# Optimization experiments

Measured on AMD Instinct MI355X. Metric: run time of the kernel, lower is better.

The kernel has to match this reference:

```python
import jax, jax.numpy as jnp
import numpy as np

D_MODEL = 1024
NUM_HEAD = 16
CHUNK = 64
NGROUPS = 2
D_HEAD = D_MODEL // NUM_HEAD
NEG = -1e30


def setup_inputs() -> dict:
    key = jax.random.key(0)
    ks = jax.random.split(key, 4)
    bs, seq = 2, 4096
    proj_dim = 3 * D_MODEL + 2 * NGROUPS * D_HEAD
    hidden = jax.random.normal(ks[0], (bs, seq, D_MODEL), jnp.float32)
    W_in = jax.random.normal(ks[1], (D_MODEL, proj_dim), jnp.float32) * (D_MODEL ** -0.5)
    # torch init: uniform_(1, chunk_size-1) then log
    gate_bias = jnp.log(jax.random.uniform(ks[2], (D_MODEL,), jnp.float32, 1.0, CHUNK - 1.0))
    rms_weight = jnp.ones((D_MODEL,), jnp.float32)
    W_out = jax.random.normal(ks[3], (D_MODEL, D_MODEL), jnp.float32) * (D_MODEL ** -0.5)
    return {"hidden_states": hidden, "rms_weight": rms_weight, "W_in": W_in,
            "gate_bias": gate_bias, "W_out": W_out}


def _scan_op(a, b):
    ga, xa = a
    gb, xb = b
    return gb * ga, gb * xa + xb


def reference(hidden_states, rms_weight, W_in, gate_bias, W_out):
    bs, seq, d = hidden_states.shape
    dh = d // NUM_HEAD
    nc = seq // CHUNK
    scale = dh ** -0.5
    rep = NUM_HEAD // NGROUPS

    shortcut = hidden_states
    # RMSNorm
    h = hidden_states * jax.lax.rsqrt(jnp.mean(hidden_states ** 2, axis=-1, keepdims=True) + 1e-6) * rms_weight
    proj = h @ W_in  # [bs, seq, 3d + 2*ng*dh]
    z, x, g, q, k = jnp.split(proj, [d, 2 * d, 3 * d, 3 * d + NGROUPS * dh], axis=-1)
    z = jax.nn.sigmoid(z)
    g = jax.nn.sigmoid(g + gate_bias)

    # repeat grouped q/k across heads (torch .repeat tiles)
    q = jnp.tile(q, (1, 1, rep))
    k = jnp.tile(k, (1, 1, rep))
    qh = q.reshape(bs, seq, NUM_HEAD, dh).transpose(0, 2, 1, 3)  # [b,h,s,dh]

    xc = x.reshape(bs, nc, CHUNK, d)
    gc = g.reshape(bs, nc, CHUNK, d)
    kc = k.reshape(bs, nc, CHUNK, d)
    g2 = jnp.concatenate([gc, gc], axis=-1)           # g.repeat(1,1,1,2)
    v = (1.0 - g2) * jnp.concatenate([xc, kc], axis=-1)
    # gated linear recurrence within each chunk: y_t = g_t*y_{t-1} + v_t
    _, xk = jax.lax.associative_scan(_scan_op, (g2, v), axis=2)

    intra_x = xk[..., :d].reshape(bs, seq, NUM_HEAD, dh).transpose(0, 2, 1, 3)  # [b,h,s,dh]
    intra_k = xk[..., d:].reshape(bs, seq, NUM_HEAD, dh).transpose(0, 2, 1, 3)

    # one kv per chunk (position 0 of each chunk, per torch [..., ::chunk_size, :])
    chunk_k = intra_k[:, :, ::CHUNK, :]  # [b,h,nc,dh]
    chunk_x = intra_x[:, :, ::CHUNK, :]

    # inter-chunk block-causal attention: query in chunk c attends kv chunks < c
    scores = jnp.einsum('bhsd,bhcd->bhsc', qh, chunk_k) * scale
    allowed = (jnp.arange(seq)[:, None] // CHUNK) > jnp.arange(nc)[None, :]  # [s,nc]
    masked = jnp.where(allowed, scores, NEG)

    # intra lse: per-token self dot product
    intra_lse = jnp.einsum('bhsd,bhsd->bhs', qh, intra_k) * scale

    # fused, numerically-stable version of flex_attention + MergeLastToken
    m = jnp.maximum(jnp.max(masked, axis=-1), intra_lse)  # [b,h,s], finite
    w = jnp.exp(masked - m[..., None])                     # zeros where masked
    intra_w = jnp.exp(intra_lse - m)
    denom = jnp.sum(w, axis=-1) + intra_w
    out = (jnp.einsum('bhsc,bhcd->bhsd', w, chunk_x) + intra_w[..., None] * intra_x) / denom[..., None]

    out = out.transpose(0, 2, 1, 3).reshape(bs, seq, d)
    return (z * out) @ W_out + shortcut
```

## Files before the change

kernel.cpp:

```cpp
#include <hip/hip_runtime.h>
#include <hip/hip_bf16.h>

typedef __bf16 bf16x8 __attribute__((ext_vector_type(8)));
typedef __bf16 bf16x4 __attribute__((ext_vector_type(4)));
typedef float  f32x4  __attribute__((ext_vector_type(4)));

#define DM 1024
#define PD 3328
#define TROWS 8192
#define SEQ 4096

__device__ __forceinline__ float sigmoidf(float x) { return 1.f / (1.f + __expf(-x)); }

__device__ __forceinline__ void gload16(const void* g, void* l) {
  __builtin_amdgcn_global_load_lds(
      (const __attribute__((address_space(1))) void*)g,
      (__attribute__((address_space(3))) void*)l, 16, 0, 0);
}

__global__ __launch_bounds__(256) void tcvt_kernel(const float* __restrict__ in,
                                                   __bf16* __restrict__ out,
                                                   int K, int N) {
  __shared__ float tile[32][33];
  int n0 = blockIdx.x * 32, k0 = blockIdx.y * 32;
  int tx = threadIdx.x, ty = threadIdx.y;
  for (int i = ty; i < 32; i += 8) tile[i][tx] = in[(size_t)(k0 + i) * N + n0 + tx];
  __syncthreads();
  for (int i = ty; i < 32; i += 8) out[(size_t)(n0 + i) * K + k0 + tx] = (__bf16)tile[tx][i];
}

__global__ __launch_bounds__(256) void rmsnorm_kernel(const float* __restrict__ hidden,
                                                      const float* __restrict__ w,
                                                      __bf16* __restrict__ hbf) {
  int r = blockIdx.x;
  int tid = threadIdx.x;
  float4 v = ((const float4*)(hidden + (size_t)r * DM))[tid];
  float ss = v.x * v.x + v.y * v.y + v.z * v.z + v.w * v.w;
#pragma unroll
  for (int off = 32; off > 0; off >>= 1) ss += __shfl_xor(ss, off);
  __shared__ float wsum[4];
  int lane = tid & 63, wid = tid >> 6;
  if (lane == 0) wsum[wid] = ss;
  __syncthreads();
  float tot = wsum[0] + wsum[1] + wsum[2] + wsum[3];
  float inv = rsqrtf(tot * (1.f / 1024.f) + 1e-6f);
  float4 wl = ((const float4*)w)[tid];
  bf16x4 o;
  o[0] = (__bf16)(v.x * inv * wl.x);
  o[1] = (__bf16)(v.y * inv * wl.y);
  o[2] = (__bf16)(v.z * inv * wl.z);
  o[3] = (__bf16)(v.w * inv * wl.w);
  *(bf16x4*)(hbf + (size_t)r * DM + tid * 4) = o;
}

template <int EPI>
__global__ __launch_bounds__(512, 4) void gemm2p(
    const __bf16* __restrict__ A, const __bf16* __restrict__ Bt,
    int N_out, int K,
    const float* __restrict__ gate_bias, const float* __restrict__ shortcut,
    float* __restrict__ outf, __bf16* __restrict__ zbf, __bf16* __restrict__ xbf,
    __bf16* __restrict__ gbf, __bf16* __restrict__ qbf, __bf16* __restrict__ kbf) {
  __shared__ __bf16 As[2][128 * 64];
  __shared__ __bf16 Bs[2][128 * 64];

  const int tid = threadIdx.x;
  const int lane = tid & 63, wid = tid >> 6;
  const int wr = wid >> 1, wc = wid & 1;

  const int nwg = gridDim.x;
  const int cpx = nwg >> 3;
  const int swz = (blockIdx.x & 7) * cpx + (blockIdx.x >> 3);
  const int ntx = N_out >> 7;
  const int m0 = (swz / ntx) << 7;
  const int n0 = (swz % ntx) << 7;

  f32x4 acc[2][4] = {};
  const int NT = K >> 6;

  const int arow0 = wr * 32 + (lane & 15);
  const int brow0 = wc * 64 + (lane & 15);

  auto stage = [&](const __bf16* src, int row0, int kt, __bf16* lbuf) {
#pragma unroll
    for (int j = 0; j < 2; ++j) {
      int off16 = tid + j * 512;
      int row = off16 >> 3, slot = off16 & 7;
      int col = (slot ^ (row & 7)) << 3;
      gload16(&src[(size_t)(row0 + row) * K + kt + col], lbuf + off16 * 8);
    }
  };
  auto fragrd = [&](const __bf16* buf, int row, int ks) -> bf16x8 {
    int s = ((ks << 2) + (lane >> 4)) ^ (row & 7);
    return *(const bf16x8*)&buf[(row << 6) + (s << 3)];
  };

  stage(A, m0, 0, &As[0][0]);
  stage(Bt, n0, 0, &Bs[0][0]);
  asm volatile("s_waitcnt vmcnt(0)" ::: "memory");
  __builtin_amdgcn_s_barrier();

  for (int t = 0; t < NT; ++t) {
    const __bf16* Ap = &As[t & 1][0];
    const __bf16* Bp = &Bs[t & 1][0];
    if (t + 1 < NT) {
      stage(A, m0, (t + 1) << 6, &As[(t + 1) & 1][0]);
      stage(Bt, n0, (t + 1) << 6, &Bs[(t + 1) & 1][0]);
    }
#pragma unroll
    for (int ks = 0; ks < 2; ++ks) {
      bf16x8 af[2], bf[4];
#pragma unroll
      for (int m = 0; m < 2; ++m) af[m] = fragrd(Ap, arow0 + m * 16, ks);
#pragma unroll
      for (int n = 0; n < 4; ++n) bf[n] = fragrd(Bp, brow0 + n * 16, ks);
      __builtin_amdgcn_s_setprio(1);
#pragma unroll
      for (int m = 0; m < 2; ++m)
#pragma unroll
        for (int n = 0; n < 4; ++n)
          acc[m][n] = __builtin_amdgcn_mfma_f32_16x16x32_bf16(af[m], bf[n], acc[m][n], 0, 0, 0);
      __builtin_amdgcn_s_setprio(0);
    }
    asm volatile("s_waitcnt vmcnt(0)" ::: "memory");
    __builtin_amdgcn_s_barrier();
  }

#pragma unroll
  for (int m = 0; m < 2; ++m) {
#pragma unroll
    for (int n = 0; n < 4; ++n) {
#pragma unroll
      for (int i = 0; i < 4; ++i) {
        int r = m0 + wr * 32 + m * 16 + ((lane >> 4) << 2) + i;
        int c = n0 + wc * 64 + n * 16 + (lane & 15);
        float v = acc[m][n][i];
        if (EPI == 1) {
          if (c < 1024)       zbf[(size_t)r * DM + c] = (__bf16)sigmoidf(v);
          else if (c < 2048)  xbf[(size_t)r * DM + (c - 1024)] = (__bf16)v;
          else if (c < 3072)  gbf[(size_t)r * DM + (c - 2048)] = (__bf16)sigmoidf(v + gate_bias[c - 2048]);
          else if (c < 3200)  qbf[(size_t)r * 128 + (c - 3072)] = (__bf16)v;
          else                kbf[(size_t)r * 128 + (c - 3200)] = (__bf16)v;
        } else {
          outf[(size_t)r * DM + c] = v + shortcut[(size_t)r * DM + c];
        }
      }
    }
  }
}

__global__ __launch_bounds__(256) void scan_kernel(const __bf16* __restrict__ g,
                                                   const __bf16* __restrict__ x,
                                                   const __bf16* __restrict__ kin,
                                                   __bf16* __restrict__ ixa,
                                                   __bf16* __restrict__ ika) {
  int bx = blockIdx.x;
  int part = bx & 3;
  int c = (bx >> 2) & 63;
  int b = bx >> 8;
  int d = part * 256 + threadIdx.x;
  size_t base = (size_t)b * SEQ + (size_t)c * 64;
  float sx = 0.f, sk = 0.f;
  for (int t = 0; t < 64; ++t) {
    size_t row = base + t;
    float gg = (float)g[row * DM + d];
    float xv = (float)x[row * DM + d];
    float kv = (float)kin[row * 128 + (d & 127)];
    sx = gg * (sx - xv) + xv;
    sk = gg * (sk - kv) + kv;
    ixa[row * DM + d] = (__bf16)sx;
    ika[row * DM + d] = (__bf16)sk;
  }
}

__global__ __launch_bounds__(256) void attn_kernel(const __bf16* __restrict__ qbf,
                                                   const __bf16* __restrict__ ixa,
                                                   const __bf16* __restrict__ ika,
                                                   const __bf16* __restrict__ zbf,
                                                   __bf16* __restrict__ y) {
  const int qt = blockIdx.x;
  const int h  = blockIdx.y;
  const int b  = blockIdx.z;
  const int tid = threadIdx.x;
  const int lane = tid & 63, wd = tid >> 6;

  __shared__ __bf16 qs[64 * 72];
  __shared__ __bf16 ck[64 * 72];
  __shared__ __bf16 cxT[64 * 72];
  __shared__ __bf16 pb[64 * 72];
  __shared__ float sc[64 * 65];
  __shared__ float rden[64], iwd[64];

  const size_t base = (size_t)b * SEQ;

  for (int i = tid; i < 512; i += 256) {
    int row = i >> 3, part = i & 7;
    *(bf16x8*)&qs[row * 72 + part * 8] =
        *(const bf16x8*)&qbf[(base + qt * 64 + row) * 128 + (h & 1) * 64 + part * 8];
    *(bf16x8*)&ck[row * 72 + part * 8] =
        *(const bf16x8*)&ika[(base + (size_t)row * 64) * DM + h * 64 + part * 8];
  }
  for (int i = tid; i < 4096; i += 256) {
    int c = i & 63, j = i >> 6;
    cxT[j * 72 + c] = ixa[(base + (size_t)c * 64) * DM + h * 64 + j];
  }
  __syncthreads();

  {
    f32x4 d4[4] = {};
#pragma unroll
    for (int kk = 0; kk < 64; kk += 32) {
      bf16x8 a = *(const bf16x8*)&qs[(wd * 16 + (lane & 15)) * 72 + kk + (lane >> 4) * 8];
#pragma unroll
      for (int ni = 0; ni < 4; ++ni) {
        bf16x8 bb = *(const bf16x8*)&ck[(ni * 16 + (lane & 15)) * 72 + kk + (lane >> 4) * 8];
        d4[ni] = __builtin_amdgcn_mfma_f32_16x16x32_bf16(a, bb, d4[ni], 0, 0, 0);
      }
    }
#pragma unroll
    for (int ni = 0; ni < 4; ++ni)
#pragma unroll
      for (int i = 0; i < 4; ++i) {
        int qrow = wd * 16 + (lane >> 4) * 4 + i;
        int c = ni * 16 + (lane & 15);
        sc[qrow * 65 + c] = 0.125f * d4[ni][i];
      }
  }

  float lse = 0.f;
  if (tid < 64) {
    const __bf16* qrow = &qbf[(base + qt * 64 + tid) * 128 + (h & 1) * 64];
    const __bf16* krow = &ika[(base + qt * 64 + tid) * DM + h * 64];
    float dot = 0.f;
#pragma unroll
    for (int p = 0; p < 8; ++p) {
      bf16x8 qa = *(const bf16x8*)&qrow[p * 8];
      bf16x8 ka = *(const bf16x8*)&krow[p * 8];
#pragma unroll
      for (int e = 0; e < 8; ++e) dot += (float)qa[e] * (float)ka[e];
    }
    lse = 0.125f * dot;
  }
  __syncthreads();

  if (tid < 64) {
    int q = tid;
    float m = lse;
    for (int c = 0; c < qt; ++c) m = fmaxf(m, sc[q * 65 + c]);
    float den = 0.f;
    for (int c = 0; c < 64; ++c) {
      float wv = (c < qt) ? __expf(sc[q * 65 + c] - m) : 0.f;
      pb[q * 72 + c] = (__bf16)wv;
      den += wv;
    }
    float iw = __expf(lse - m);
    den += iw;
    rden[q] = 1.f / den;
    iwd[q] = iw;
  }
  __syncthreads();

  {
    f32x4 d4[4] = {};
#pragma unroll
    for (int kk = 0; kk < 64; kk += 32) {
      bf16x8 a = *(const bf16x8*)&pb[(wd * 16 + (lane & 15)) * 72 + kk + (lane >> 4) * 8];
#pragma unroll
      for (int ni = 0; ni < 4; ++ni) {
        bf16x8 bb = *(const bf16x8*)&cxT[(ni * 16 + (lane & 15)) * 72 + kk + (lane >> 4) * 8];
        d4[ni] = __builtin_amdgcn_mfma_f32_16x16x32_bf16(a, bb, d4[ni], 0, 0, 0);
      }
    }
#pragma unroll
    for (int ni = 0; ni < 4; ++ni)
#pragma unroll
      for (int i = 0; i < 4; ++i) {
        int qrow = wd * 16 + (lane >> 4) * 4 + i;
        int j = ni * 16 + (lane & 15);
        size_t srow = base + qt * 64 + qrow;
        float ix = (float)ixa[srow * DM + h * 64 + j];
        float outv = (d4[ni][i] + iwd[qrow] * ix) * rden[qrow];
        float zv = (float)zbf[srow * DM + h * 64 + j];
        y[srow * DM + h * 64 + j] = (__bf16)(outv * zv);
      }
  }
}

extern "C" void kernel_launch(void* const* d_in, const int* in_sizes, int n_in,
                              void* d_out, int out_size, void* d_ws, size_t ws_size,
                              hipStream_t stream) {
  const float* hidden = (const float*)d_in[0];
  const float* rmsw   = (const float*)d_in[1];
  const float* Win    = (const float*)d_in[2];
  const float* gbias  = (const float*)d_in[3];
  const float* Wout   = (const float*)d_in[4];
  float* out = (float*)d_out;

  char* ws = (char*)d_ws;
  size_t o = 0;
  auto alloc = [&](size_t bytes) { char* p = ws + o; o += (bytes + 255) & ~(size_t)255; return p; };
  __bf16* WinT  = (__bf16*)alloc((size_t)PD * DM * 2);
  __bf16* WoutT = (__bf16*)alloc((size_t)DM * DM * 2);
  __bf16* hy    = (__bf16*)alloc((size_t)TROWS * DM * 2);
  __bf16* zbf   = (__bf16*)alloc((size_t)TROWS * DM * 2);
  __bf16* xbf   = (__bf16*)alloc((size_t)TROWS * DM * 2);
  __bf16* gbf   = (__bf16*)alloc((size_t)TROWS * DM * 2);
  __bf16* qbf   = (__bf16*)alloc((size_t)TROWS * 128 * 2);
  __bf16* kbf   = (__bf16*)alloc((size_t)TROWS * 128 * 2);
  __bf16* ixa   = (__bf16*)alloc((size_t)TROWS * DM * 2);
  __bf16* ika   = (__bf16*)alloc((size_t)TROWS * DM * 2);

  tcvt_kernel<<<dim3(PD / 32, DM / 32), dim3(32, 8), 0, stream>>>(Win, WinT, DM, PD);
  tcvt_kernel<<<dim3(DM / 32, DM / 32), dim3(32, 8), 0, stream>>>(Wout, WoutT, DM, DM);
  rmsnorm_kernel<<<TROWS, 256, 0, stream>>>(hidden, rmsw, hy);
  gemm2p<1><<<dim3((TROWS / 128) * (PD / 128)), 512, 0, stream>>>(
      hy, WinT, PD, DM, gbias, nullptr, nullptr, zbf, xbf, gbf, qbf, kbf);
  scan_kernel<<<512, 256, 0, stream>>>(gbf, xbf, kbf, ixa, ika);
  attn_kernel<<<dim3(64, 16, 2), 256, 0, stream>>>(qbf, ixa, ika, zbf, hy);
  gemm2p<0><<<dim3((TROWS / 128) * (DM / 128)), 512, 0, stream>>>(
      hy, WoutT, DM, DM, nullptr, hidden, out, nullptr, nullptr, nullptr, nullptr, nullptr);
}
```

Measured before the change: 197.3 us.

## Replace GEMM with 256-row tiles and a four-phase half-K software pipeline

```diff
diff --git a/kernel.cpp b/kernel.cpp
--- a/kernel.cpp
+++ b/kernel.cpp
@@ -10,12 +10,30 @@
 #define TROWS 8192
 #define SEQ 4096
 
+template <int N> struct ic_t { static constexpr int v = N; };
+
 __device__ __forceinline__ float sigmoidf(float x) { return 1.f / (1.f + __expf(-x)); }
 
 __device__ __forceinline__ void gload16(const void* g, void* l) {
   __builtin_amdgcn_global_load_lds(
       (const __attribute__((address_space(1))) void*)g,
       (__attribute__((address_space(3))) void*)l, 16, 0, 0);
+}
+
+template <int N>
+__device__ __forceinline__ void vmwait() {
+  if constexpr (N == 0)      asm volatile("s_waitcnt vmcnt(0)" ::: "memory");
+  else if constexpr (N == 3) asm volatile("s_waitcnt vmcnt(3)" ::: "memory");
+  else if constexpr (N == 4) asm volatile("s_waitcnt vmcnt(4)" ::: "memory");
+  else if constexpr (N == 6) asm volatile("s_waitcnt vmcnt(6)" ::: "memory");
+  else if constexpr (N == 8) asm volatile("s_waitcnt vmcnt(8)" ::: "memory");
+  else static_assert(N == 0 || N == 3 || N == 4 || N == 6 || N == 8, "add case");
+}
+
+__device__ __forceinline__ void wgbar() {
+  asm volatile("" ::: "memory");
+  __builtin_amdgcn_s_barrier();
+  asm volatile("" ::: "memory");
 }
 
 __global__ __launch_bounds__(256) void tcvt_kernel(const float* __restrict__ in,
@@ -53,87 +71,138 @@
   *(bf16x4*)(hbf + (size_t)r * DM + tid * 4) = o;
 }
 
-template <int EPI>
-__global__ __launch_bounds__(512, 4) void gemm2p(
+template <int BM, int BN, int EPI>
+__global__ __launch_bounds__(512, 2) void gemm4p(
     const __bf16* __restrict__ A, const __bf16* __restrict__ Bt,
     int N_out, int K,
     const float* __restrict__ gate_bias, const float* __restrict__ shortcut,
     float* __restrict__ outf, __bf16* __restrict__ zbf, __bf16* __restrict__ xbf,
     __bf16* __restrict__ gbf, __bf16* __restrict__ qbf, __bf16* __restrict__ kbf) {
-  __shared__ __bf16 As[2][128 * 64];
-  __shared__ __bf16 Bs[2][128 * 64];
+  constexpr int NF = BN / 64;
+  constexpr int NG = NF / 2;
+  constexpr int SA = BM / 128;
+  constexpr int SB = BN / 128;
+  constexpr int FULL = 2 * (SA + SB);
+  constexpr int HALF = SA + SB;
+
+  __shared__ __bf16 As[2][2][BM * 32];
+  __shared__ __bf16 Bs[2][2][BN * 32];
 
   const int tid = threadIdx.x;
   const int lane = tid & 63, wid = tid >> 6;
-  const int wr = wid >> 1, wc = wid & 1;
-
-  const int nwg = gridDim.x;
-  const int cpx = nwg >> 3;
+  const int wm = wid >> 2, wn = wid & 3;
+  const int lr = lane & 15, hh = lane >> 4;
+
+  const int nwg = gridDim.x, cpx = nwg >> 3;
   const int swz = (blockIdx.x & 7) * cpx + (blockIdx.x >> 3);
-  const int ntx = N_out >> 7;
-  const int m0 = (swz / ntx) << 7;
-  const int n0 = (swz % ntx) << 7;
-
-  f32x4 acc[2][4] = {};
+  const int ntx = N_out / BN;
+  const int m0 = (swz / ntx) * BM, n0 = (swz % ntx) * BN;
+
   const int NT = K >> 6;
-
-  const int arow0 = wr * 32 + (lane & 15);
-  const int brow0 = wc * 64 + (lane & 15);
-
-  auto stage = [&](const __bf16* src, int row0, int kt, __bf16* lbuf) {
+  f32x4 acc[8][NF] = {};
+  bf16x8 afr[8];
+
+  const int arow = wm * 128 + lr;
+  const int brow = wn * (BN / 4) + lr;
+
+  auto stage_half = [&](const __bf16* src, int rows_unused, int row0, int kcol,
+                        __bf16* hp, int nloads) {
+    (void)rows_unused;
 #pragma unroll
     for (int j = 0; j < 2; ++j) {
-      int off16 = tid + j * 512;
-      int row = off16 >> 3, slot = off16 & 7;
-      int col = (slot ^ (row & 7)) << 3;
-      gload16(&src[(size_t)(row0 + row) * K + kt + col], lbuf + off16 * 8);
+      if (j < nloads) {
+        int c = tid + j * 512;
+        int p = c >> 3, phi = c & 7;
+        int lam = phi ^ (p & 7);
+        int r = 2 * p + (lam >> 2), s = lam & 3;
+        gload16(&src[(size_t)(row0 + r) * K + kcol + s * 8], hp + c * 8);
+      }
     }
   };
-  auto fragrd = [&](const __bf16* buf, int row, int ks) -> bf16x8 {
-    int s = ((ks << 2) + (lane >> 4)) ^ (row & 7);
-    return *(const bf16x8*)&buf[(row << 6) + (s << 3)];
+  auto fragrd = [&](const __bf16* hp, int r) -> bf16x8 {
+    int p = r >> 1;
+    int phi = (((r & 1) << 2) | hh) ^ (p & 7);
+    return *(const bf16x8*)&hp[(p << 6) + (phi << 3)];
   };
 
-  stage(A, m0, 0, &As[0][0]);
-  stage(Bt, n0, 0, &Bs[0][0]);
-  asm volatile("s_waitcnt vmcnt(0)" ::: "memory");
-  __builtin_amdgcn_s_barrier();
-
-  for (int t = 0; t < NT; ++t) {
-    const __bf16* Ap = &As[t & 1][0];
-    const __bf16* Bp = &Bs[t & 1][0];
-    if (t + 1 < NT) {
-      stage(A, m0, (t + 1) << 6, &As[(t + 1) & 1][0]);
-      stage(Bt, n0, (t + 1) << 6, &Bs[(t + 1) & 1][0]);
-    }
-#pragma unroll
-    for (int ks = 0; ks < 2; ++ks) {
-      bf16x8 af[2], bf[4];
-#pragma unroll
-      for (int m = 0; m < 2; ++m) af[m] = fragrd(Ap, arow0 + m * 16, ks);
-#pragma unroll
-      for (int n = 0; n < 4; ++n) bf[n] = fragrd(Bp, brow0 + n * 16, ks);
-      __builtin_amdgcn_s_setprio(1);
-#pragma unroll
-      for (int m = 0; m < 2; ++m)
-#pragma unroll
-        for (int n = 0; n < 4; ++n)
-          acc[m][n] = __builtin_amdgcn_mfma_f32_16x16x32_bf16(af[m], bf[n], acc[m][n], 0, 0, 0);
-      __builtin_amdgcn_s_setprio(0);
-    }
-    asm volatile("s_waitcnt vmcnt(0)" ::: "memory");
-    __builtin_amdgcn_s_barrier();
-  }
-
-#pragma unroll
-  for (int m = 0; m < 2; ++m) {
-#pragma unroll
-    for (int n = 0; n < 4; ++n) {
+  stage_half(A,  0, m0, 0,  &As[0][0][0], SA);
+  stage_half(Bt, 0, n0, 0,  &Bs[0][0][0], SB);
+  stage_half(A,  0, m0, 32, &As[0][1][0], SA);
+  stage_half(Bt, 0, n0, 32, &Bs[0][1][0], SB);
+  stage_half(A,  0, m0, 64, &As[1][0][0], SA);
+  stage_half(Bt, 0, n0, 64, &Bs[1][0][0], SB);
+  vmwait<FULL>();
+  wgbar();
+
+  auto phase = [&](int t, auto kkc, auto ngc, auto stg, auto vmw) {
+    constexpr int kk = decltype(kkc)::v;
+    constexpr int ngi = decltype(ngc)::v;
+    const __bf16* Ah = &As[t & 1][kk][0];
+    const __bf16* Bh = &Bs[t & 1][kk][0];
+    if constexpr (ngi == 0) {
+#pragma unroll
+      for (int mf = 0; mf < 8; ++mf) afr[mf] = fragrd(Ah, arow + mf * 16);
+    }
+    bf16x8 bfr[NG];
+#pragma unroll
+    for (int g = 0; g < NG; ++g) bfr[g] = fragrd(Bh, brow + (ngi * NG + g) * 16);
+    stg();
+    vmw();
+    wgbar();
+    __builtin_amdgcn_s_setprio(1);
+#pragma unroll
+    for (int mf = 0; mf < 8; ++mf)
+#pragma unroll
+      for (int g = 0; g < NG; ++g)
+        acc[mf][ngi * NG + g] = __builtin_amdgcn_mfma_f32_16x16x32_bf16(
+            afr[mf], bfr[g], acc[mf][ngi * NG + g], 0, 0, 0);
+    __builtin_amdgcn_s_setprio(0);
+    wgbar();
+  };
+  auto nostg = [] {};
+  auto nowait = [] {};
+
+  for (int t = 0; t + 2 < NT; ++t) {
+    int k1 = ((t + 1) << 6) + 32, k2 = (t + 2) << 6;
+    phase(t, ic_t<0>{}, ic_t<0>{},
+          [&] { stage_half(A, 0, m0, k1, &As[(t + 1) & 1][1][0], SA); }, nowait);
+    phase(t, ic_t<0>{}, ic_t<1>{},
+          [&] { stage_half(Bt, 0, n0, k1, &Bs[(t + 1) & 1][1][0], SB); },
+          [] { vmwait<FULL>(); });
+    phase(t, ic_t<1>{}, ic_t<0>{},
+          [&] { stage_half(A, 0, m0, k2, &As[t & 1][0][0], SA); }, nowait);
+    phase(t, ic_t<1>{}, ic_t<1>{},
+          [&] { stage_half(Bt, 0, n0, k2, &Bs[t & 1][0][0], SB); },
+          [] { vmwait<FULL>(); });
+  }
+  {
+    int t = NT - 2;
+    int k1 = ((t + 1) << 6) + 32;
+    phase(t, ic_t<0>{}, ic_t<0>{},
+          [&] { stage_half(A, 0, m0, k1, &As[(t + 1) & 1][1][0], SA); }, nowait);
+    phase(t, ic_t<0>{}, ic_t<1>{},
+          [&] { stage_half(Bt, 0, n0, k1, &Bs[(t + 1) & 1][1][0], SB); },
+          [] { vmwait<FULL>(); });
+    phase(t, ic_t<1>{}, ic_t<0>{}, nostg, nowait);
+    phase(t, ic_t<1>{}, ic_t<1>{}, nostg, [] { vmwait<HALF>(); });
+  }
+  {
+    int t = NT - 1;
+    phase(t, ic_t<0>{}, ic_t<0>{}, nostg, nowait);
+    phase(t, ic_t<0>{}, ic_t<1>{}, nostg, [] { vmwait<0>(); });
+    phase(t, ic_t<1>{}, ic_t<0>{}, nostg, nowait);
+    phase(t, ic_t<1>{}, ic_t<1>{}, nostg, nowait);
+  }
+
+#pragma unroll
+  for (int mf = 0; mf < 8; ++mf) {
+#pragma unroll
+    for (int nf = 0; nf < NF; ++nf) {
 #pragma unroll
       for (int i = 0; i < 4; ++i) {
-        int r = m0 + wr * 32 + m * 16 + ((lane >> 4) << 2) + i;
-        int c = n0 + wc * 64 + n * 16 + (lane & 15);
-        float v = acc[m][n][i];
+        int r = m0 + wm * 128 + mf * 16 + (hh << 2) + i;
+        int c = n0 + wn * (BN / 4) + nf * 16 + lr;
+        float v = acc[mf][nf][i];
         if (EPI == 1) {
           if (c < 1024)       zbf[(size_t)r * DM + c] = (__bf16)sigmoidf(v);
           else if (c < 2048)  xbf[(size_t)r * DM + (c - 1024)] = (__bf16)v;
@@ -312,10 +381,10 @@
   tcvt_kernel<<<dim3(PD / 32, DM / 32), dim3(32, 8), 0, stream>>>(Win, WinT, DM, PD);
   tcvt_kernel<<<dim3(DM / 32, DM / 32), dim3(32, 8), 0, stream>>>(Wout, WoutT, DM, DM);
   rmsnorm_kernel<<<TROWS, 256, 0, stream>>>(hidden, rmsw, hy);
-  gemm2p<1><<<dim3((TROWS / 128) * (PD / 128)), 512, 0, stream>>>(
+  gemm4p<256, 256, 1><<<dim3((TROWS / 256) * (PD / 256)), 512, 0, stream>>>(
       hy, WinT, PD, DM, gbias, nullptr, nullptr, zbf, xbf, gbf, qbf, kbf);
   scan_kernel<<<512, 256, 0, stream>>>(gbf, xbf, kbf, ixa, ika);
   attn_kernel<<<dim3(64, 16, 2), 256, 0, stream>>>(qbf, ixa, ika, zbf, hy);
-  gemm2p<0><<<dim3((TROWS / 128) * (DM / 128)), 512, 0, stream>>>(
+  gemm4p<256, 128, 0><<<dim3((TROWS / 256) * (DM / 128)), 512, 0, stream>>>(
       hy, WoutT, DM, DM, nullptr, hidden, out, nullptr, nullptr, nullptr, nullptr, nullptr);
 }
```

New measurement: 218.9 us. 1.11x slower.

## Pre-transpose chunk x in scan and parallelize attention softmax across all threads

Applied to the files above, without the earlier changes.

```diff
diff --git a/kernel.cpp b/kernel.cpp
--- a/kernel.cpp
+++ b/kernel.cpp
@@ -152,7 +152,8 @@
                                                    const __bf16* __restrict__ x,
                                                    const __bf16* __restrict__ kin,
                                                    __bf16* __restrict__ ixa,
-                                                   __bf16* __restrict__ ika) {
+                                                   __bf16* __restrict__ ika,
+                                                   __bf16* __restrict__ cxtg) {
   int bx = blockIdx.x;
   int part = bx & 3;
   int c = (bx >> 2) & 63;
@@ -169,12 +170,14 @@
     sk = gg * (sk - kv) + kv;
     ixa[row * DM + d] = (__bf16)sx;
     ika[row * DM + d] = (__bf16)sk;
+    if (t == 0) cxtg[((size_t)b * DM + d) * 64 + c] = (__bf16)sx;
   }
 }
 
 __global__ __launch_bounds__(256) void attn_kernel(const __bf16* __restrict__ qbf,
                                                    const __bf16* __restrict__ ixa,
                                                    const __bf16* __restrict__ ika,
+                                                   const __bf16* __restrict__ cxtg,
                                                    const __bf16* __restrict__ zbf,
                                                    __bf16* __restrict__ y) {
   const int qt = blockIdx.x;
@@ -188,7 +191,7 @@
   __shared__ __bf16 cxT[64 * 72];
   __shared__ __bf16 pb[64 * 72];
   __shared__ float sc[64 * 65];
-  __shared__ float rden[64], iwd[64];
+  __shared__ float rden[64], iwd[64], rlse[64];
 
   const size_t base = (size_t)b * SEQ;
 
@@ -198,10 +201,8 @@
         *(const bf16x8*)&qbf[(base + qt * 64 + row) * 128 + (h & 1) * 64 + part * 8];
     *(bf16x8*)&ck[row * 72 + part * 8] =
         *(const bf16x8*)&ika[(base + (size_t)row * 64) * DM + h * 64 + part * 8];
-  }
-  for (int i = tid; i < 4096; i += 256) {
-    int c = i & 63, j = i >> 6;
-    cxT[j * 72 + c] = ixa[(base + (size_t)c * 64) * DM + h * 64 + j];
+    *(bf16x8*)&cxT[row * 72 + part * 8] =
+        *(const bf16x8*)&cxtg[((size_t)b * DM + h * 64 + row) * 64 + part * 8];
   }
   __syncthreads();
 
@@ -226,36 +227,53 @@
       }
   }
 
-  float lse = 0.f;
-  if (tid < 64) {
-    const __bf16* qrow = &qbf[(base + qt * 64 + tid) * 128 + (h & 1) * 64];
-    const __bf16* krow = &ika[(base + qt * 64 + tid) * DM + h * 64];
+  {
+    int s = tid >> 2, p = tid & 3;
+    const __bf16* krow = &ika[(base + qt * 64 + s) * DM + h * 64 + p * 16];
     float dot = 0.f;
 #pragma unroll
-    for (int p = 0; p < 8; ++p) {
-      bf16x8 qa = *(const bf16x8*)&qrow[p * 8];
-      bf16x8 ka = *(const bf16x8*)&krow[p * 8];
+    for (int half = 0; half < 2; ++half) {
+      bf16x8 qa = *(const bf16x8*)&qs[s * 72 + p * 16 + half * 8];
+      bf16x8 ka = *(const bf16x8*)&krow[half * 8];
 #pragma unroll
       for (int e = 0; e < 8; ++e) dot += (float)qa[e] * (float)ka[e];
     }
-    lse = 0.125f * dot;
-  }
-  __syncthreads();
-
-  if (tid < 64) {
-    int q = tid;
-    float m = lse;
-    for (int c = 0; c < qt; ++c) m = fmaxf(m, sc[q * 65 + c]);
+    dot += __shfl_xor(dot, 1);
+    dot += __shfl_xor(dot, 2);
+    if (p == 0) rlse[s] = 0.125f * dot;
+  }
+  __syncthreads();
+
+  {
+    int s = tid >> 2, p = tid & 3;
+    float lse = rlse[s];
+    float m = -1e30f;
+#pragma unroll
+    for (int k = 0; k < 16; ++k) {
+      int c = p * 16 + k;
+      if (c < qt) m = fmaxf(m, sc[s * 65 + c]);
+    }
+    m = fmaxf(m, __shfl_xor(m, 1));
+    m = fmaxf(m, __shfl_xor(m, 2));
+    m = fmaxf(m, lse);
     float den = 0.f;
-    for (int c = 0; c < 64; ++c) {
-      float wv = (c < qt) ? __expf(sc[q * 65 + c] - m) : 0.f;
-      pb[q * 72 + c] = (__bf16)wv;
+    bf16x8 w0, w1;
+#pragma unroll
+    for (int k = 0; k < 16; ++k) {
+      int c = p * 16 + k;
+      float wv = (c < qt) ? __expf(sc[s * 65 + c] - m) : 0.f;
+      if (k < 8) w0[k] = (__bf16)wv; else w1[k - 8] = (__bf16)wv;
       den += wv;
     }
+    *(bf16x8*)&pb[s * 72 + p * 16] = w0;
+    *(bf16x8*)&pb[s * 72 + p * 16 + 8] = w1;
+    den += __shfl_xor(den, 1);
+    den += __shfl_xor(den, 2);
     float iw = __expf(lse - m);
-    den += iw;
-    rden[q] = 1.f / den;
-    iwd[q] = iw;
+    if (p == 0) {
+      rden[s] = 1.f / (den + iw);
+      iwd[s] = iw;
+    }
   }
   __syncthreads();
 
@@ -308,14 +326,15 @@
   __bf16* kbf   = (__bf16*)alloc((size_t)TROWS * 128 * 2);
   __bf16* ixa   = (__bf16*)alloc((size_t)TROWS * DM * 2);
   __bf16* ika   = (__bf16*)alloc((size_t)TROWS * DM * 2);
+  __bf16* cxtg  = (__bf16*)alloc((size_t)2 * DM * 64 * 2);
 
   tcvt_kernel<<<dim3(PD / 32, DM / 32), dim3(32, 8), 0, stream>>>(Win, WinT, DM, PD);
   tcvt_kernel<<<dim3(DM / 32, DM / 32), dim3(32, 8), 0, stream>>>(Wout, WoutT, DM, DM);
   rmsnorm_kernel<<<TROWS, 256, 0, stream>>>(hidden, rmsw, hy);
   gemm2p<1><<<dim3((TROWS / 128) * (PD / 128)), 512, 0, stream>>>(
       hy, WinT, PD, DM, gbias, nullptr, nullptr, zbf, xbf, gbf, qbf, kbf);
-  scan_kernel<<<512, 256, 0, stream>>>(gbf, xbf, kbf, ixa, ika);
-  attn_kernel<<<dim3(64, 16, 2), 256, 0, stream>>>(qbf, ixa, ika, zbf, hy);
+  scan_kernel<<<512, 256, 0, stream>>>(gbf, xbf, kbf, ixa, ika, cxtg);
+  attn_kernel<<<dim3(64, 16, 2), 256, 0, stream>>>(qbf, ixa, ika, cxtg, zbf, hy);
   gemm2p<0><<<dim3((TROWS / 128) * (DM / 128)), 512, 0, stream>>>(
       hy, WoutT, DM, DM, nullptr, hidden, out, nullptr, nullptr, nullptr, nullptr, nullptr);
 }
```

After: 174.5 us. 11.6% less time.
